# Kernel tuning notes

Hardware: AMD Instinct MI355X
Metric: run time of the kernel (lower is better)

## Reference

```python
import jax, jax.numpy as jnp
import numpy as np

N = 512  # DFT size, fixed by the module


def _dft_weights():
    # W[h, j] = exp(-2i*pi*j*h/N), same as the torch init loop
    h = np.arange(N).reshape(N, 1).astype(np.float64)
    j = np.arange(N).reshape(1, N).astype(np.float64)
    ang = -2.0 * np.pi * (h * j) / N
    return np.cos(ang).astype(np.float32), np.sin(ang).astype(np.float32)


def setup_inputs() -> dict:
    key = jax.random.key(0)
    k1, k2 = jax.random.split(key)
    shape = (8, 16, 256, N)  # (batch, channels, doppler, range_samples)
    x_re = jax.random.normal(k1, shape, dtype=jnp.float32)
    x_im = jax.random.normal(k2, shape, dtype=jnp.float32)
    w_re, w_im = _dft_weights()
    return {
        "x_re": x_re,
        "x_im": x_im,
        "w_re": jnp.asarray(w_re),
        "w_im": jnp.asarray(w_im),
    }


def reference(x_re, x_im, w_re, w_im):
    # CplxLinear without bias: y = x @ W^T, complex.
    # y_re = x_re @ Wr^T - x_im @ Wi^T ; y_im = x_re @ Wi^T + x_im @ Wr^T
    y_re = jnp.einsum('bcdj,hj->bcdh', x_re, w_re) - jnp.einsum('bcdj,hj->bcdh', x_im, w_im)
    y_im = jnp.einsum('bcdj,hj->bcdh', x_re, w_im) + jnp.einsum('bcdj,hj->bcdh', x_im, w_re)
    # stack real/imag on trailing axis (equivalent to torch.view_as_real layout)
    return jnp.stack([y_re, y_im], axis=-1)
```

## Files before the change

### kernel.cpp

```cpp
#include <hip/hip_runtime.h>

typedef __bf16 bf16_t;
typedef __bf16 bf16x8 __attribute__((ext_vector_type(8)));
typedef float f32x4 __attribute__((ext_vector_type(4)));
typedef unsigned int u32x4 __attribute__((ext_vector_type(4)));

#define KDIM 512
#define NDIM 512
#define BM 128
#define BN 128
#define BK 32
#define WSTRIDE 40

__device__ __forceinline__ void gld_lds16(const float* g, float* lds_uniform) {
  __builtin_amdgcn_global_load_lds(
      (const __attribute__((address_space(1))) void*)g,
      (__attribute__((address_space(3))) void*)lds_uniform, 16, 0, 0);
}

__device__ __forceinline__ bf16x8 neg8(bf16x8 v) {
  union { bf16x8 b; u32x4 u; } x;
  x.b = v;
  x.u = x.u ^ 0x80008000u;
  return x.b;
}

__device__ __forceinline__ bf16x8 afrag(const float* ldsx, int r, int h4) {
  const int base = r * 8;
  const int sw = r & 7;
  const float4 a = *(const float4*)(ldsx + 4 * (base + ((2 * h4) ^ sw)));
  const float4 b = *(const float4*)(ldsx + 4 * (base + ((2 * h4 + 1) ^ sw)));
  bf16x8 f;
  f[0] = (__bf16)a.x; f[1] = (__bf16)a.y; f[2] = (__bf16)a.z; f[3] = (__bf16)a.w;
  f[4] = (__bf16)b.x; f[5] = (__bf16)b.y; f[6] = (__bf16)b.z; f[7] = (__bf16)b.w;
  return f;
}

__global__ __launch_bounds__(256, 2) void dft_cgemm_kernel(
    const float* __restrict__ xr, const float* __restrict__ xi,
    const float* __restrict__ wre, const float* __restrict__ wim,
    float* __restrict__ out) {
  __shared__ __align__(16) float lds_xr[BM * BK];
  __shared__ __align__(16) float lds_xi[BM * BK];
  __shared__ __align__(16) bf16_t lds_wr[BN * WSTRIDE];
  __shared__ __align__(16) bf16_t lds_wi[BN * WSTRIDE];

  const int t = threadIdx.x;
  const int lane = t & 63;
  const int wv = t >> 6;
  const int m0 = blockIdx.y * BM;
  const int n0 = blockIdx.x * BN;

  const int wm = (wv >> 1) * 64;
  const int wn = (wv & 1) * 64;
  const int l16 = lane & 15;
  const int h4 = lane >> 4;

  const int wrow = t >> 1;
  const int wcol = (t & 1) * 16;

  f32x4 acc_re[4][4], acc_im[4][4];
#pragma unroll
  for (int i = 0; i < 4; ++i)
#pragma unroll
    for (int j = 0; j < 4; ++j) {
      acc_re[i][j] = (f32x4){0.f, 0.f, 0.f, 0.f};
      acc_im[i][j] = (f32x4){0.f, 0.f, 0.f, 0.f};
    }

  for (int k0 = 0; k0 < KDIM; k0 += BK) {
#pragma unroll
    for (int it = 0; it < 4; ++it) {
      const int S = it * 256 + t;
      const int row = S >> 3;
      const int g = (S & 7) ^ (row & 7);
      const size_t goff = (size_t)(m0 + row) * KDIM + k0 + g * 4;
      float* dst_r = lds_xr + 4 * (it * 256 + wv * 64);
      float* dst_i = lds_xi + 4 * (it * 256 + wv * 64);
      gld_lds16(xr + goff, dst_r);
      gld_lds16(xi + goff, dst_i);
    }
    {
      const float* gwr = wre + (size_t)(n0 + wrow) * KDIM + k0 + wcol;
      const float* gwi = wim + (size_t)(n0 + wrow) * KDIM + k0 + wcol;
      const float4 a0 = ((const float4*)gwr)[0];
      const float4 a1 = ((const float4*)gwr)[1];
      const float4 a2 = ((const float4*)gwr)[2];
      const float4 a3 = ((const float4*)gwr)[3];
      const float4 b0 = ((const float4*)gwi)[0];
      const float4 b1 = ((const float4*)gwi)[1];
      const float4 b2 = ((const float4*)gwi)[2];
      const float4 b3 = ((const float4*)gwi)[3];
      bf16x8 pr0, pr1, pi0, pi1;
      pr0[0]=(__bf16)a0.x; pr0[1]=(__bf16)a0.y; pr0[2]=(__bf16)a0.z; pr0[3]=(__bf16)a0.w;
      pr0[4]=(__bf16)a1.x; pr0[5]=(__bf16)a1.y; pr0[6]=(__bf16)a1.z; pr0[7]=(__bf16)a1.w;
      pr1[0]=(__bf16)a2.x; pr1[1]=(__bf16)a2.y; pr1[2]=(__bf16)a2.z; pr1[3]=(__bf16)a2.w;
      pr1[4]=(__bf16)a3.x; pr1[5]=(__bf16)a3.y; pr1[6]=(__bf16)a3.z; pr1[7]=(__bf16)a3.w;
      pi0[0]=(__bf16)b0.x; pi0[1]=(__bf16)b0.y; pi0[2]=(__bf16)b0.z; pi0[3]=(__bf16)b0.w;
      pi0[4]=(__bf16)b1.x; pi0[5]=(__bf16)b1.y; pi0[6]=(__bf16)b1.z; pi0[7]=(__bf16)b1.w;
      pi1[0]=(__bf16)b2.x; pi1[1]=(__bf16)b2.y; pi1[2]=(__bf16)b2.z; pi1[3]=(__bf16)b2.w;
      pi1[4]=(__bf16)b3.x; pi1[5]=(__bf16)b3.y; pi1[6]=(__bf16)b3.z; pi1[7]=(__bf16)b3.w;
      *(bf16x8*)(lds_wr + wrow * WSTRIDE + wcol)     = pr0;
      *(bf16x8*)(lds_wr + wrow * WSTRIDE + wcol + 8) = pr1;
      *(bf16x8*)(lds_wi + wrow * WSTRIDE + wcol)     = pi0;
      *(bf16x8*)(lds_wi + wrow * WSTRIDE + wcol + 8) = pi1;
    }
    __syncthreads();

    bf16x8 ar[4], ai[4], br[4], bi[4], nbi[4];
#pragma unroll
    for (int mi = 0; mi < 4; ++mi) {
      const int r = wm + mi * 16 + l16;
      ar[mi] = afrag(lds_xr, r, h4);
      ai[mi] = afrag(lds_xi, r, h4);
    }
#pragma unroll
    for (int ni = 0; ni < 4; ++ni) {
      const int r = wn + ni * 16 + l16;
      br[ni] = *(const bf16x8*)(lds_wr + r * WSTRIDE + h4 * 8);
      bi[ni] = *(const bf16x8*)(lds_wi + r * WSTRIDE + h4 * 8);
      nbi[ni] = neg8(bi[ni]);
    }
#pragma unroll
    for (int mi = 0; mi < 4; ++mi) {
#pragma unroll
      for (int ni = 0; ni < 4; ++ni) {
        acc_re[mi][ni] = __builtin_amdgcn_mfma_f32_16x16x32_bf16(ar[mi], br[ni], acc_re[mi][ni], 0, 0, 0);
        acc_im[mi][ni] = __builtin_amdgcn_mfma_f32_16x16x32_bf16(ar[mi], bi[ni], acc_im[mi][ni], 0, 0, 0);
        acc_re[mi][ni] = __builtin_amdgcn_mfma_f32_16x16x32_bf16(ai[mi], nbi[ni], acc_re[mi][ni], 0, 0, 0);
        acc_im[mi][ni] = __builtin_amdgcn_mfma_f32_16x16x32_bf16(ai[mi], br[ni], acc_im[mi][ni], 0, 0, 0);
      }
    }
    __syncthreads();
  }

#pragma unroll
  for (int mi = 0; mi < 4; ++mi) {
#pragma unroll
    for (int r = 0; r < 4; ++r) {
      const int m = m0 + wm + mi * 16 + h4 * 4 + r;
#pragma unroll
      for (int ni = 0; ni < 4; ++ni) {
        const int h = n0 + wn + ni * 16 + l16;
        float2 v;
        v.x = acc_re[mi][ni][r];
        v.y = acc_im[mi][ni][r];
        *(float2*)(out + ((size_t)m * NDIM + h) * 2) = v;
      }
    }
  }
}

extern "C" void kernel_launch(void* const* d_in, const int* in_sizes, int n_in,
                              void* d_out, int out_size, void* d_ws, size_t ws_size,
                              hipStream_t stream) {
  const float* xr  = (const float*)d_in[0];
  const float* xi  = (const float*)d_in[1];
  const float* wre = (const float*)d_in[2];
  const float* wim = (const float*)d_in[3];
  float* out = (float*)d_out;

  const int M = in_sizes[0] / KDIM;
  dim3 grid(NDIM / BN, M / BM);
  dim3 block(256);
  dft_cgemm_kernel<<<grid, block, 0, stream>>>(xr, xi, wre, wim, out);
}
```

Baseline: 295.5 us.

## Remap blocks per XCD and store W tiles in fragment-order LDS layout

Changes the grid to 1D with 1024 blocks and remaps block index so that the four N-tiles of each M row-block land on the same XCD, improving L2 reuse of the x tiles across XCDs. It also replaces the padded W LDS layout with a fragment-ordered one, so each thread writes and the MFMA B-fragment reads are contiguous 16-byte slots without padding. The grid size is now hardcoded for the fixed input shape (M=32768).

```diff
diff --git a/kernel.cpp b/kernel.cpp
--- a/kernel.cpp
+++ b/kernel.cpp
@@ -10,7 +10,6 @@
 #define BM 128
 #define BN 128
 #define BK 32
-#define WSTRIDE 40
 
 __device__ __forceinline__ void gld_lds16(const float* g, float* lds_uniform) {
   __builtin_amdgcn_global_load_lds(
@@ -36,28 +35,39 @@
   return f;
 }
 
+__device__ __forceinline__ bf16x8 pack8(float4 a, float4 b) {
+  bf16x8 f;
+  f[0] = (__bf16)a.x; f[1] = (__bf16)a.y; f[2] = (__bf16)a.z; f[3] = (__bf16)a.w;
+  f[4] = (__bf16)b.x; f[5] = (__bf16)b.y; f[6] = (__bf16)b.z; f[7] = (__bf16)b.w;
+  return f;
+}
+
 __global__ __launch_bounds__(256, 2) void dft_cgemm_kernel(
     const float* __restrict__ xr, const float* __restrict__ xi,
     const float* __restrict__ wre, const float* __restrict__ wim,
     float* __restrict__ out) {
   __shared__ __align__(16) float lds_xr[BM * BK];
   __shared__ __align__(16) float lds_xi[BM * BK];
-  __shared__ __align__(16) bf16_t lds_wr[BN * WSTRIDE];
-  __shared__ __align__(16) bf16_t lds_wi[BN * WSTRIDE];
+  __shared__ __align__(16) bf16_t lds_wr[BN * BK];
+  __shared__ __align__(16) bf16_t lds_wi[BN * BK];
 
   const int t = threadIdx.x;
   const int lane = t & 63;
   const int wv = t >> 6;
-  const int m0 = blockIdx.y * BM;
-  const int n0 = blockIdx.x * BN;
+
+  const int b = blockIdx.x;
+  const int xcd = b & 7;
+  const int sidx = b >> 3;
+  const int m0 = (xcd * 32 + (sidx >> 2)) * BM;
+  const int n0 = (sidx & 3) * BN;
 
   const int wm = (wv >> 1) * 64;
   const int wn = (wv & 1) * 64;
   const int l16 = lane & 15;
   const int h4 = lane >> 4;
 
-  const int wrow = t >> 1;
-  const int wcol = (t & 1) * 16;
+  const int wt15 = t & 15;
+  const int wg = (t >> 4) & 3;
 
   f32x4 acc_re[4][4], acc_im[4][4];
 #pragma unroll
@@ -80,30 +90,18 @@
       gld_lds16(xr + goff, dst_r);
       gld_lds16(xi + goff, dst_i);
     }
-    {
-      const float* gwr = wre + (size_t)(n0 + wrow) * KDIM + k0 + wcol;
-      const float* gwi = wim + (size_t)(n0 + wrow) * KDIM + k0 + wcol;
-      const float4 a0 = ((const float4*)gwr)[0];
-      const float4 a1 = ((const float4*)gwr)[1];
-      const float4 a2 = ((const float4*)gwr)[2];
-      const float4 a3 = ((const float4*)gwr)[3];
-      const float4 b0 = ((const float4*)gwi)[0];
-      const float4 b1 = ((const float4*)gwi)[1];
-      const float4 b2 = ((const float4*)gwi)[2];
-      const float4 b3 = ((const float4*)gwi)[3];
-      bf16x8 pr0, pr1, pi0, pi1;
-      pr0[0]=(__bf16)a0.x; pr0[1]=(__bf16)a0.y; pr0[2]=(__bf16)a0.z; pr0[3]=(__bf16)a0.w;
-      pr0[4]=(__bf16)a1.x; pr0[5]=(__bf16)a1.y; pr0[6]=(__bf16)a1.z; pr0[7]=(__bf16)a1.w;
-      pr1[0]=(__bf16)a2.x; pr1[1]=(__bf16)a2.y; pr1[2]=(__bf16)a2.z; pr1[3]=(__bf16)a2.w;
-      pr1[4]=(__bf16)a3.x; pr1[5]=(__bf16)a3.y; pr1[6]=(__bf16)a3.z; pr1[7]=(__bf16)a3.w;
-      pi0[0]=(__bf16)b0.x; pi0[1]=(__bf16)b0.y; pi0[2]=(__bf16)b0.z; pi0[3]=(__bf16)b0.w;
-      pi0[4]=(__bf16)b1.x; pi0[5]=(__bf16)b1.y; pi0[6]=(__bf16)b1.z; pi0[7]=(__bf16)b1.w;
-      pi1[0]=(__bf16)b2.x; pi1[1]=(__bf16)b2.y; pi1[2]=(__bf16)b2.z; pi1[3]=(__bf16)b2.w;
-      pi1[4]=(__bf16)b3.x; pi1[5]=(__bf16)b3.y; pi1[6]=(__bf16)b3.z; pi1[7]=(__bf16)b3.w;
-      *(bf16x8*)(lds_wr + wrow * WSTRIDE + wcol)     = pr0;
-      *(bf16x8*)(lds_wr + wrow * WSTRIDE + wcol + 8) = pr1;
-      *(bf16x8*)(lds_wi + wrow * WSTRIDE + wcol)     = pi0;
-      *(bf16x8*)(lds_wi + wrow * WSTRIDE + wcol + 8) = pi1;
+#pragma unroll
+    for (int c = 0; c < 2; ++c) {
+      const int row = (c * 4 + wv) * 16 + wt15;
+      const float* gr = wre + (size_t)(n0 + row) * KDIM + k0 + wg * 8;
+      const float* gi = wim + (size_t)(n0 + row) * KDIM + k0 + wg * 8;
+      const float4 r0 = ((const float4*)gr)[0];
+      const float4 r1 = ((const float4*)gr)[1];
+      const float4 i0 = ((const float4*)gi)[0];
+      const float4 i1 = ((const float4*)gi)[1];
+      const int slot = c * 256 + t;
+      *(bf16x8*)(lds_wr + slot * 8) = pack8(r0, r1);
+      *(bf16x8*)(lds_wi + slot * 8) = pack8(i0, i1);
     }
     __syncthreads();
 
@@ -116,9 +114,9 @@
     }
 #pragma unroll
     for (int ni = 0; ni < 4; ++ni) {
-      const int r = wn + ni * 16 + l16;
-      br[ni] = *(const bf16x8*)(lds_wr + r * WSTRIDE + h4 * 8);
-      bi[ni] = *(const bf16x8*)(lds_wi + r * WSTRIDE + h4 * 8);
+      const int slot = ((wn >> 4) + ni) * 64 + h4 * 16 + l16;
+      br[ni] = *(const bf16x8*)(lds_wr + slot * 8);
+      bi[ni] = *(const bf16x8*)(lds_wi + slot * 8);
       nbi[ni] = neg8(bi[ni]);
     }
 #pragma unroll
@@ -160,8 +158,7 @@
   const float* wim = (const float*)d_in[3];
   float* out = (float*)d_out;
 
-  const int M = in_sizes[0] / KDIM;
-  dim3 grid(NDIM / BN, M / BM);
+  dim3 grid(1024);
   dim3 block(256);
   dft_cgemm_kernel<<<grid, block, 0, stream>>>(xr, xi, wre, wim, out);
 }
```

After: 291.5 us. Within noise of the previous version (-1.3%).
